# Kernel tuning notes

Hardware: AMD Instinct MI355X
Metric: run time of the kernel (lower is better)

## Reference

```python
import jax, jax.numpy as jnp
import numpy as np
import math

B, T, M, C, H = 4, 1024, 256, 512, 8
HD = C // H
NEG = -1e30


def setup_inputs() -> dict:
    key = jax.random.key(0)
    ks = jax.random.split(key, 16)
    s = 1.0 / math.sqrt(C)
    inp = {
        'x': jax.random.normal(ks[0], (B, T, C), jnp.float32),
        'y': jax.random.normal(ks[1], (B, M, C), jnp.float32),
        'attn_x_mask': jnp.tril(jnp.ones((T, T), bool))[None, None],  # causal (1,1,T,T)
        'Wqkv_x': jax.random.normal(ks[2], (C, 3 * C), jnp.float32) * s,
        'bqkv_x': jnp.zeros((3 * C,), jnp.float32),
        'Wqkv_y': jax.random.normal(ks[3], (C, 3 * C), jnp.float32) * s,
        'bqkv_y': jnp.zeros((3 * C,), jnp.float32),
        'w4x': jax.random.normal(ks[4], (H, HD), jnp.float32) * math.sqrt(1.0 / C / 3),
        'w4y': jax.random.normal(ks[5], (H, HD), jnp.float32) * math.sqrt(1.0 / C / 3),
        'w4xy': jax.random.normal(ks[6], (H, HD), jnp.float32) * math.sqrt(1.0 / C / 3),
        'Wgs': jax.random.normal(ks[7], (C, C), jnp.float32) * s,
        'bgs': jnp.zeros((C,), jnp.float32),
        'Wgc': jax.random.normal(ks[8], (C, C), jnp.float32) * s,
        'bgc': jnp.zeros((C,), jnp.float32),
        'Wp': jax.random.normal(ks[9], (C, C), jnp.float32) * s,
        'bp': jnp.zeros((C,), jnp.float32),
    }
    return inp


def _heads(t):
    b, n, c = t.shape
    return t.reshape(b, n, H, HD).transpose(0, 2, 1, 3)  # (B,H,N,HD)


def reference(x, y, attn_x_mask, Wqkv_x, bqkv_x, Wqkv_y, bqkv_y,
              w4x, w4y, w4xy, Wgs, bgs, Wgc, bgc, Wp, bp):
    q_x, k_x, v_x = [_heads(t) for t in jnp.split(x @ Wqkv_x + bqkv_x, 3, axis=-1)]
    q_y, k_y, v_y = [_heads(t) for t in jnp.split(y @ Wqkv_y + bqkv_y, 3, axis=-1)]
    scale = 1.0 / math.sqrt(HD)

    # additive bias attention: catt1 (per query-x), catt2 (per key-y), catt3 (bilinear)
    catt1 = jnp.einsum('bhtd,hd->bht', q_x, w4x)[..., :, None]          # (B,H,T,1)
    catt2 = jnp.einsum('bhmd,hd->bhm', q_y, w4y)[:, :, None, :]          # (B,H,1,M)
    catt3 = jnp.einsum('bhtd,bhmd->bhtm', q_x * w4xy[None, :, None, :], k_y) * scale
    catt = catt1 + catt2 + catt3                                         # (B,H,T,M)

    catt_x2y = jax.nn.softmax(catt, axis=-1)
    catt_y2x = jax.nn.softmax(catt, axis=-2)

    cval_x2y = jnp.einsum('bhtm,bhmd->bhtd', catt_x2y, v_y)
    cval_x2y = cval_x2y.transpose(0, 2, 1, 3).reshape(B, T, C)

    # product-of-attentions: (T,M) @ (M,T) -> (T,T)
    chain = jnp.einsum('bhtm,bhsm->bhts', catt_x2y, catt_y2x) * (1.0 / math.sqrt(M))
    chain = jnp.where(attn_x_mask, chain, NEG)
    chain = jax.nn.softmax(chain, axis=-1)
    cval_y2x = jnp.einsum('bhts,bhsd->bhtd', chain, v_x)
    cval_y2x = cval_y2x.transpose(0, 2, 1, 3).reshape(B, T, C)

    cval = cval_x2y + cval_y2x + x

    # masked self-attention
    satt = jnp.einsum('bhtd,bhsd->bhts', q_x, k_x) * scale
    satt = jnp.where(attn_x_mask, satt, NEG)
    satt = jax.nn.softmax(satt, axis=-1)
    sval = jnp.einsum('bhts,bhsd->bhtd', satt, v_x).transpose(0, 2, 1, 3).reshape(B, T, C)

    sgate = jax.nn.sigmoid(sval @ Wgs + bgs)
    cgate = jax.nn.sigmoid(cval @ Wgc + bgc)
    out = (sgate * cval + cgate * sval) @ Wp + bp
    return out
```

## Files before the change

kernel.cpp:

```cpp
#include <hip/hip_runtime.h>
#include <hip/hip_bf16.h>

typedef __hip_bfloat16 bf16;
using f4 = __attribute__((ext_vector_type(4))) float;
using s8 = __attribute__((ext_vector_type(8))) short;
using s4 = __attribute__((ext_vector_type(4))) short;

__device__ __forceinline__ void storeOut(float* p, float v) { *p = v; }
__device__ __forceinline__ void storeOut(bf16* p, float v) { *p = __float2bfloat16(v); }
__device__ __forceinline__ short bfs(float x) { return __builtin_bit_cast(short, __float2bfloat16(x)); }

constexpr int B_ = 4, T_ = 1024, M_ = 256, C_ = 512, H_ = 8, HD_ = 64, C3_ = 1536;

#define MFMA16(a, b, c) __builtin_amdgcn_mfma_f32_16x16x32_bf16((a), (b), (c), 0, 0, 0)

__global__ __launch_bounds__(256) void prep_kernel(
    const float* __restrict__ Wqkv_x, const float* __restrict__ Wqkv_y,
    const float* __restrict__ Wgs, const float* __restrict__ Wgc, const float* __restrict__ Wp,
    const float* __restrict__ x, const float* __restrict__ y,
    bf16* __restrict__ WT_x, bf16* __restrict__ WT_y, bf16* __restrict__ WT_gs,
    bf16* __restrict__ WT_gc, bf16* __restrict__ WT_p,
    bf16* __restrict__ x_bf, bf16* __restrict__ y_bf)
{
    __shared__ float Ls[64][65];
    const int tid = threadIdx.x;
    const int bid = blockIdx.x;
    if (bid < 576) {
        const float* W; bf16* WT; int N, t;
        if (bid < 192)      { W = Wqkv_x; WT = WT_x;  N = C3_; t = bid; }
        else if (bid < 384) { W = Wqkv_y; WT = WT_y;  N = C3_; t = bid - 192; }
        else if (bid < 448) { W = Wgs;    WT = WT_gs; N = C_;  t = bid - 384; }
        else if (bid < 512) { W = Wgc;    WT = WT_gc; N = C_;  t = bid - 448; }
        else                { W = Wp;     WT = WT_p;  N = C_;  t = bid - 512; }
        const int K = C_;
        const int tw = N >> 6;
        const int n0 = (t % tw) * 64, k0 = (t / tw) * 64;
        for (int i = tid; i < 1024; i += 256) {
            int kr = i >> 4, ng = i & 15;
            float4 v = *(const float4*)&W[(size_t)(k0 + kr) * N + n0 + ng * 4];
            Ls[ng * 4 + 0][kr] = v.x; Ls[ng * 4 + 1][kr] = v.y;
            Ls[ng * 4 + 2][kr] = v.z; Ls[ng * 4 + 3][kr] = v.w;
        }
        __syncthreads();
        for (int i = tid; i < 512; i += 256) {
            int n = i >> 3, kg = i & 7;
            s8 r;
            #pragma unroll
            for (int j = 0; j < 8; ++j) r[j] = bfs(Ls[n][kg * 8 + j]);
            *(s8*)&WT[(size_t)(n0 + n) * K + k0 + kg * 8] = r;
        }
    } else if (bid < 1600) {
        int i = (bid - 576) * 2048 + tid * 8;
        s8 r;
        #pragma unroll
        for (int j = 0; j < 8; ++j) r[j] = bfs(x[i + j]);
        *(s8*)&x_bf[i] = r;
    } else {
        int i = (bid - 1600) * 2048 + tid * 8;
        s8 r;
        #pragma unroll
        for (int j = 0; j < 8; ++j) r[j] = bfs(y[i + j]);
        *(s8*)&y_bf[i] = r;
    }
}

__global__ __launch_bounds__(256) void qwcatt_kernel(
    const bf16* __restrict__ qkv_x, const bf16* __restrict__ qkv_y,
    const float* __restrict__ w4x, const float* __restrict__ w4y,
    const float* __restrict__ w4xy,
    float* __restrict__ catt1b, float* __restrict__ catt2b, bf16* __restrict__ qw)
{
    const int bid = blockIdx.x;
    const int tid = threadIdx.x;
    if (bid < 160) {
        int i = bid * 256 + tid;
        const bf16* row; const float* w; float* out; int oi;
        if (i < 32768) {
            int bh = i >> 10, t = i & 1023, b = bh >> 3, h = bh & 7;
            row = qkv_x + (size_t)(b * T_ + t) * C3_ + h * HD_;
            w = w4x + h * HD_; out = catt1b; oi = i;
        } else {
            int j = i - 32768;
            int bh = j >> 8, m = j & 255, b = bh >> 3, h = bh & 7;
            row = qkv_y + (size_t)(b * M_ + m) * C3_ + h * HD_;
            w = w4y + h * HD_; out = catt2b; oi = j;
        }
        float s = 0.f;
        #pragma unroll
        for (int d = 0; d < HD_; ++d) s = fmaf(__bfloat162float(row[d]), w[d], s);
        out[oi] = s;
    } else {
        int o = ((bid - 160) * 256 + tid) * 8;
        int row = o >> 9, c = o & 511;
        const bf16* src = qkv_x + (size_t)row * C3_ + c;
        s8 r;
        #pragma unroll
        for (int j = 0; j < 8; ++j) r[j] = bfs(__bfloat162float(src[j]) * w4xy[c + j]);
        *(s8*)&qw[o] = r;
    }
}

template <typename OT>
__global__ __launch_bounds__(256) void gemm_staged_kernel(
    const bf16* __restrict__ A, const bf16* __restrict__ WT, const float* __restrict__ bias,
    OT* __restrict__ Cmat, int N, int K)
{
    __shared__ short Asb[128][72];
    __shared__ short Bsb[64][72];
    const int tid = threadIdx.x;
    const int wave = tid >> 6, lane = tid & 63;
    const int quad = lane >> 4, l16 = lane & 15;
    const int n0 = blockIdx.y * 64, m0 = blockIdx.x * 128;
    f4 acc[2][4];
    #pragma unroll
    for (int mt = 0; mt < 2; ++mt)
        #pragma unroll
        for (int nt = 0; nt < 4; ++nt) acc[mt][nt] = (f4)0.f;

    for (int k0 = 0; k0 < K; k0 += 64) {
        #pragma unroll
        for (int tl = 0; tl < 4; ++tl) {
            int g = tid + tl * 256, row = g >> 3, grp = g & 7;
            *(s8*)&Asb[row][grp * 8] = *(const s8*)&A[(size_t)(m0 + row) * K + k0 + grp * 8];
        }
        #pragma unroll
        for (int tl = 0; tl < 2; ++tl) {
            int g = tid + tl * 256, n = g >> 3, grp = g & 7;
            *(s8*)&Bsb[n][grp * 8] = *(const s8*)&WT[(size_t)(n0 + n) * K + k0 + grp * 8];
        }
        __syncthreads();
        #pragma unroll
        for (int ks = 0; ks < 2; ++ks) {
            s8 a0 = *(const s8*)&Asb[wave * 32 + l16][ks * 32 + quad * 8];
            s8 a1 = *(const s8*)&Asb[wave * 32 + 16 + l16][ks * 32 + quad * 8];
            #pragma unroll
            for (int nt = 0; nt < 4; ++nt) {
                s8 bv = *(const s8*)&Bsb[nt * 16 + l16][ks * 32 + quad * 8];
                acc[0][nt] = MFMA16(a0, bv, acc[0][nt]);
                acc[1][nt] = MFMA16(a1, bv, acc[1][nt]);
            }
        }
        __syncthreads();
    }
    #pragma unroll
    for (int mt = 0; mt < 2; ++mt)
        #pragma unroll
        for (int nt = 0; nt < 4; ++nt) {
            int col = n0 + nt * 16 + l16;
            float bb = bias[col];
            #pragma unroll
            for (int reg = 0; reg < 4; ++reg) {
                int row = m0 + wave * 32 + mt * 16 + quad * 4 + reg;
                storeOut(&Cmat[(size_t)row * N + col], acc[mt][nt][reg] + bb);
            }
        }
}

__global__ __launch_bounds__(256) void catt3_kernel(
    const bf16* __restrict__ qw, const bf16* __restrict__ qkv_y,
    const float* __restrict__ catt1, const float* __restrict__ catt2,
    float* __restrict__ catt, float* __restrict__ psum)
{
    __shared__ float redc[4][64];
    const int tid = threadIdx.x;
    const int wave = tid >> 6, lane = tid & 63;
    const int quad = lane >> 4, l16 = lane & 15;
    const int bh = blockIdx.x, b = bh >> 3, h = bh & 7;
    const int m0 = blockIdx.y * 64, t0 = blockIdx.z * 64;
    f4 sc[4];
    #pragma unroll
    for (int nt = 0; nt < 4; ++nt) sc[nt] = (f4)0.f;
    const bf16* ap = qw + (size_t)(b * T_ + t0 + wave * 16 + l16) * C_ + h * HD_ + quad * 8;
    const bf16* bp = qkv_y + (size_t)(b * M_ + m0 + l16) * C3_ + C_ + h * HD_ + quad * 8;
    #pragma unroll
    for (int k0 = 0; k0 < 64; k0 += 32) {
        s8 a = *(const s8*)(ap + k0);
        #pragma unroll
        for (int nt = 0; nt < 4; ++nt) {
            s8 bv = *(const s8*)(bp + (size_t)nt * 16 * C3_ + k0);
            sc[nt] = MFMA16(a, bv, sc[nt]);
        }
    }
    float csloc[4];
    #pragma unroll
    for (int nt = 0; nt < 4; ++nt) {
        int m = m0 + nt * 16 + l16;
        float c2 = catt2[bh * M_ + m];
        float es = 0.f;
        #pragma unroll
        for (int reg = 0; reg < 4; ++reg) {
            int t = t0 + wave * 16 + quad * 4 + reg;
            float v = sc[nt][reg] * 0.125f + catt1[bh * T_ + t] + c2;
            catt[((size_t)bh * T_ + t) * M_ + m] = v;
            es += __expf(v);
        }
        es += __shfl_xor(es, 16);
        es += __shfl_xor(es, 32);
        csloc[nt] = es;
    }
    if (quad == 0) {
        #pragma unroll
        for (int nt = 0; nt < 4; ++nt) redc[wave][nt * 16 + l16] = csloc[nt];
    }
    __syncthreads();
    if (tid < 64) {
        float s = redc[0][tid] + redc[1][tid] + redc[2][tid] + redc[3][tid];
        psum[((size_t)bh * 16 + (t0 >> 6)) * M_ + m0 + tid] = s;
    }
}

__global__ __launch_bounds__(256) void colfin_vtrans_kernel(
    const float* __restrict__ psum, float* __restrict__ colinv,
    const bf16* __restrict__ qkv_x, const bf16* __restrict__ qkv_y,
    bf16* __restrict__ vTx, bf16* __restrict__ vTy)
{
    __shared__ short Ls[64][68];
    const int tid = threadIdx.x;
    int bid = blockIdx.x;
    if (bid < 32) {
        const int bh = bid, m = tid;
        float s = 0.f;
        #pragma unroll
        for (int ch = 0; ch < 16; ++ch) s += psum[(bh * 16 + ch) * M_ + m];
        colinv[bh * M_ + m] = 1.f / s;
        return;
    }
    bid -= 32;
    const bf16* qkv; bf16* vT; int Nrows, bh, t0;
    if (bid < 512) { qkv = qkv_x; vT = vTx; Nrows = T_; bh = bid >> 4; t0 = (bid & 15) * 64; }
    else { bid -= 512; qkv = qkv_y; vT = vTy; Nrows = M_; bh = bid >> 2; t0 = (bid & 3) * 64; }
    const int b = bh >> 3, h = bh & 7;
    for (int i = tid; i < 4096; i += 256) {
        int tl = i >> 6, d = i & 63;
        Ls[d][tl] = __builtin_bit_cast(short,
            qkv[(size_t)(b * Nrows + t0 + tl) * C3_ + 2 * C_ + h * HD_ + d]);
    }
    __syncthreads();
    for (int i = tid; i < 4096; i += 256) {
        int d = i >> 6, tl = i & 63;
        vT[((size_t)bh * 64 + d) * Nrows + t0 + tl] = __builtin_bit_cast(bf16, Ls[d][tl]);
    }
}

__global__ __launch_bounds__(256) void rowsoft_kernel(
    const float* __restrict__ catt, const float* __restrict__ colinv,
    bf16* __restrict__ x2y, bf16* __restrict__ y2x)
{
    const int wave = threadIdx.x >> 6, lane = threadIdx.x & 63;
    const int row = blockIdx.x * 4 + wave;
    const int bh = row >> 10;
    const float* p = catt + (size_t)row * M_;
    float e[4];
    float s = 0.f;
    #pragma unroll
    for (int j = 0; j < 4; ++j) { e[j] = __expf(p[j * 64 + lane]); s += e[j]; }
    for (int off = 1; off < 64; off <<= 1) s += __shfl_xor(s, off);
    float inv = 1.f / s;
    #pragma unroll
    for (int j = 0; j < 4; ++j) {
        int m = j * 64 + lane;
        x2y[(size_t)row * M_ + m] = __float2bfloat16(e[j] * inv);
        y2x[(size_t)row * M_ + m] = __float2bfloat16(e[j] * colinv[bh * M_ + m]);
    }
}

__global__ __launch_bounds__(512) void flash6_kernel(
    const bf16* __restrict__ x2y, const bf16* __restrict__ y2x,
    const bf16* __restrict__ vTx, const bf16* __restrict__ vTy,
    const bf16* __restrict__ qkv_x, const float* __restrict__ x,
    float* __restrict__ cval, bf16* __restrict__ cval_bf,
    float* __restrict__ sval, bf16* __restrict__ sval_bf)
{
    __shared__ short Kc[64][264];
    __shared__ short Ksf[64][72];
    __shared__ short Vb[64][72];
    __shared__ short Ps[8][16][68];
    const int tid = threadIdx.x;
    const int wave = tid >> 6, lane = tid & 63;
    const int quad = lane >> 4, l16 = lane & 15;
    const int bh = blockIdx.x, b = bh >> 3, h = bh & 7;
    const int p = blockIdx.y;
    const int jt = (wave < 4) ? p : (15 - p);
    const int rb = jt * 64 + (wave & 3) * 16;
    const int nst = 16 - p;

    s8 qc[8], qs[2];
    {
        const bf16* qp = x2y + (size_t)(bh * T_ + rb + l16) * M_ + quad * 8;
        #pragma unroll
        for (int f = 0; f < 8; ++f) qc[f] = *(const s8*)(qp + f * 32);
        const bf16* qsp = qkv_x + (size_t)(b * T_ + rb + l16) * C3_ + h * HD_ + quad * 8;
        qs[0] = *(const s8*)qsp;
        qs[1] = *(const s8*)(qsp + 32);
    }

    f4 ocv[4];
    #pragma unroll
    for (int dt = 0; dt < 4; ++dt) ocv[dt] = (f4)0.f;
    {
        const bf16* vb = vTy + (size_t)(bh * 64 + l16) * M_ + quad * 8;
        #pragma unroll
        for (int f = 0; f < 8; ++f)
            #pragma unroll
            for (int dt = 0; dt < 4; ++dt) {
                s8 bv = *(const s8*)(vb + (size_t)dt * 16 * M_ + f * 32);
                ocv[dt] = MFMA16(qc[f], bv, ocv[dt]);
            }
    }

    f4 oc[4], os_[4];
    float lc[4] = {0.f, 0.f, 0.f, 0.f}, ls_[4] = {0.f, 0.f, 0.f, 0.f};
    #pragma unroll
    for (int dt = 0; dt < 4; ++dt) { oc[dt] = (f4)0.f; os_[dt] = (f4)0.f; }

    #pragma unroll
    for (int tl = 0; tl < 4; ++tl) {
        int g = tid + tl * 512, row = g >> 5, grp = g & 31;
        *(s8*)&Kc[row][grp * 8] = *(const s8*)&y2x[(size_t)(bh * T_ + row) * M_ + grp * 8];
    }
    {
        int row = tid >> 3, grp = tid & 7;
        *(s8*)&Ksf[row][grp * 8] =
            *(const s8*)&qkv_x[(size_t)(b * T_ + row) * C3_ + C_ + h * HD_ + grp * 8];
        *(s8*)&Vb[row][grp * 8] = *(const s8*)&vTx[(size_t)(bh * 64 + row) * T_ + grp * 8];
    }
    __syncthreads();

    for (int st = 0; st < nst; ++st) {
        const int s0 = st * 64;
        const bool pf = (st + 1) < nst;
        s8 kcp[4], ksp, vp;
        if (pf) {
            const int sn = s0 + 64;
            #pragma unroll
            for (int tl = 0; tl < 4; ++tl) {
                int g = tid + tl * 512, row = g >> 5, grp = g & 31;
                kcp[tl] = *(const s8*)&y2x[(size_t)(bh * T_ + sn + row) * M_ + grp * 8];
            }
            int row = tid >> 3, grp = tid & 7;
            ksp = *(const s8*)&qkv_x[(size_t)(b * T_ + sn + row) * C3_ + C_ + h * HD_ + grp * 8];
            vp = *(const s8*)&vTx[(size_t)(bh * 64 + row) * T_ + sn + grp * 8];
        }
        if (st <= jt) {
            f4 sc[4];
            #pragma unroll
            for (int nt = 0; nt < 4; ++nt) sc[nt] = (f4)0.f;
            #pragma unroll
            for (int f = 0; f < 8; ++f)
                #pragma unroll
                for (int nt = 0; nt < 4; ++nt) {
                    s8 bv = *(const s8*)&Kc[nt * 16 + l16][f * 32 + quad * 8];
                    sc[nt] = MFMA16(qc[f], bv, sc[nt]);
                }
            f4 ss[4];
            #pragma unroll
            for (int nt = 0; nt < 4; ++nt) ss[nt] = (f4)0.f;
            #pragma unroll
            for (int f = 0; f < 2; ++f)
                #pragma unroll
                for (int nt = 0; nt < 4; ++nt) {
                    s8 bv = *(const s8*)&Ksf[nt * 16 + l16][f * 32 + quad * 8];
                    ss[nt] = MFMA16(qs[f], bv, ss[nt]);
                }
            #pragma unroll
            for (int reg = 0; reg < 4; ++reg) {
                const int t_g = rb + quad * 4 + reg;
                #pragma unroll
                for (int nt = 0; nt < 4; ++nt) {
                    float pv = (s0 + nt * 16 + l16 <= t_g) ? __expf(sc[nt][reg] * (1.f / 16.f)) : 0.f;
                    lc[reg] += pv;
                    Ps[wave][quad * 4 + reg][nt * 16 + l16] = bfs(pv);
                }
            }
            #pragma unroll
            for (int ks = 0; ks < 2; ++ks) {
                const short* pp = &Ps[wave][l16][ks * 32 + quad * 8];
                s4 alo = *(const s4*)pp;
                s4 ahi = *(const s4*)(pp + 4);
                s8 a;
                a[0] = alo[0]; a[1] = alo[1]; a[2] = alo[2]; a[3] = alo[3];
                a[4] = ahi[0]; a[5] = ahi[1]; a[6] = ahi[2]; a[7] = ahi[3];
                #pragma unroll
                for (int dt = 0; dt < 4; ++dt) {
                    s8 bv = *(const s8*)&Vb[dt * 16 + l16][ks * 32 + quad * 8];
                    oc[dt] = MFMA16(a, bv, oc[dt]);
                }
            }
            #pragma unroll
            for (int reg = 0; reg < 4; ++reg) {
                const int t_g = rb + quad * 4 + reg;
                #pragma unroll
                for (int nt = 0; nt < 4; ++nt) {
                    float pv = (s0 + nt * 16 + l16 <= t_g) ? __expf(ss[nt][reg] * 0.125f) : 0.f;
                    ls_[reg] += pv;
                    Ps[wave][quad * 4 + reg][nt * 16 + l16] = bfs(pv);
                }
            }
            #pragma unroll
            for (int ks = 0; ks < 2; ++ks) {
                const short* pp = &Ps[wave][l16][ks * 32 + quad * 8];
                s4 alo = *(const s4*)pp;
                s4 ahi = *(const s4*)(pp + 4);
                s8 a;
                a[0] = alo[0]; a[1] = alo[1]; a[2] = alo[2]; a[3] = alo[3];
                a[4] = ahi[0]; a[5] = ahi[1]; a[6] = ahi[2]; a[7] = ahi[3];
                #pragma unroll
                for (int dt = 0; dt < 4; ++dt) {
                    s8 bv = *(const s8*)&Vb[dt * 16 + l16][ks * 32 + quad * 8];
                    os_[dt] = MFMA16(a, bv, os_[dt]);
                }
            }
        }
        __syncthreads();
        if (pf) {
            #pragma unroll
            for (int tl = 0; tl < 4; ++tl) {
                int g = tid + tl * 512, row = g >> 5, grp = g & 31;
                *(s8*)&Kc[row][grp * 8] = kcp[tl];
            }
            int row = tid >> 3, grp = tid & 7;
            *(s8*)&Ksf[row][grp * 8] = ksp;
            *(s8*)&Vb[row][grp * 8] = vp;
        }
        __syncthreads();
    }

    #pragma unroll
    for (int reg = 0; reg < 4; ++reg) {
        float l1 = lc[reg], l2 = ls_[reg];
        l1 += __shfl_xor(l1, 1); l1 += __shfl_xor(l1, 2);
        l1 += __shfl_xor(l1, 4); l1 += __shfl_xor(l1, 8);
        l2 += __shfl_xor(l2, 1); l2 += __shfl_xor(l2, 2);
        l2 += __shfl_xor(l2, 4); l2 += __shfl_xor(l2, 8);
        const float i1 = 1.f / l1, i2 = 1.f / l2;
        const int t = rb + quad * 4 + reg;
        #pragma unroll
        for (int dt = 0; dt < 4; ++dt) {
            size_t idx = (size_t)(b * T_ + t) * C_ + h * HD_ + dt * 16 + l16;
            float cv = ocv[dt][reg] + oc[dt][reg] * i1 + x[idx];
            cval[idx] = cv;
            cval_bf[idx] = __float2bfloat16(cv);
            float sv = os_[dt][reg] * i2;
            sval[idx] = sv;
            sval_bf[idx] = __float2bfloat16(sv);
        }
    }
}

__global__ __launch_bounds__(256) void gatefuse_kernel(
    const bf16* __restrict__ svalb, const bf16* __restrict__ cvalb,
    const bf16* __restrict__ WTgs, const bf16* __restrict__ WTgc,
    const float* __restrict__ bgs, const float* __restrict__ bgc,
    const float* __restrict__ cval, const float* __restrict__ sval,
    bf16* __restrict__ gated)
{
    __shared__ short Sb[128][72], Cb[128][72], W1b[64][72], W2b[64][72];
    const int tid = threadIdx.x;
    const int wave = tid >> 6, lane = tid & 63;
    const int quad = lane >> 4, l16 = lane & 15;
    const int n0 = blockIdx.y * 64, m0 = blockIdx.x * 128;
    f4 aS[2][4], aC[2][4];
    #pragma unroll
    for (int mt = 0; mt < 2; ++mt)
        #pragma unroll
        for (int nt = 0; nt < 4; ++nt) { aS[mt][nt] = (f4)0.f; aC[mt][nt] = (f4)0.f; }

    for (int k0 = 0; k0 < C_; k0 += 64) {
        #pragma unroll
        for (int tl = 0; tl < 4; ++tl) {
            int g = tid + tl * 256, row = g >> 3, grp = g & 7;
            *(s8*)&Sb[row][grp * 8] = *(const s8*)&svalb[(size_t)(m0 + row) * C_ + k0 + grp * 8];
            *(s8*)&Cb[row][grp * 8] = *(const s8*)&cvalb[(size_t)(m0 + row) * C_ + k0 + grp * 8];
        }
        #pragma unroll
        for (int tl = 0; tl < 2; ++tl) {
            int g = tid + tl * 256, n = g >> 3, grp = g & 7;
            *(s8*)&W1b[n][grp * 8] = *(const s8*)&WTgs[(size_t)(n0 + n) * C_ + k0 + grp * 8];
            *(s8*)&W2b[n][grp * 8] = *(const s8*)&WTgc[(size_t)(n0 + n) * C_ + k0 + grp * 8];
        }
        __syncthreads();
        #pragma unroll
        for (int ks = 0; ks < 2; ++ks) {
            s8 s0f = *(const s8*)&Sb[wave * 32 + l16][ks * 32 + quad * 8];
            s8 s1f = *(const s8*)&Sb[wave * 32 + 16 + l16][ks * 32 + quad * 8];
            s8 c0f = *(const s8*)&Cb[wave * 32 + l16][ks * 32 + quad * 8];
            s8 c1f = *(const s8*)&Cb[wave * 32 + 16 + l16][ks * 32 + quad * 8];
            #pragma unroll
            for (int nt = 0; nt < 4; ++nt) {
                s8 w1 = *(const s8*)&W1b[nt * 16 + l16][ks * 32 + quad * 8];
                s8 w2 = *(const s8*)&W2b[nt * 16 + l16][ks * 32 + quad * 8];
                aS[0][nt] = MFMA16(s0f, w1, aS[0][nt]);
                aS[1][nt] = MFMA16(s1f, w1, aS[1][nt]);
                aC[0][nt] = MFMA16(c0f, w2, aC[0][nt]);
                aC[1][nt] = MFMA16(c1f, w2, aC[1][nt]);
            }
        }
        __syncthreads();
    }
    #pragma unroll
    for (int mt = 0; mt < 2; ++mt)
        #pragma unroll
        for (int nt = 0; nt < 4; ++nt) {
            int col = n0 + nt * 16 + l16;
            float b1 = bgs[col], b2 = bgc[col];
            #pragma unroll
            for (int reg = 0; reg < 4; ++reg) {
                int row = m0 + wave * 32 + mt * 16 + quad * 4 + reg;
                size_t idx = (size_t)row * C_ + col;
                float gs = 1.f / (1.f + __expf(-(aS[mt][nt][reg] + b1)));
                float gc = 1.f / (1.f + __expf(-(aC[mt][nt][reg] + b2)));
                gated[idx] = __float2bfloat16(gs * cval[idx] + gc * sval[idx]);
            }
        }
}

extern "C" void kernel_launch(void* const* d_in, const int* in_sizes, int n_in,
                              void* d_out, int out_size, void* d_ws, size_t ws_size,
                              hipStream_t stream)
{
    const float* x      = (const float*)d_in[0];
    const float* y      = (const float*)d_in[1];
    const float* Wqkv_x = (const float*)d_in[3];
    const float* bqkv_x = (const float*)d_in[4];
    const float* Wqkv_y = (const float*)d_in[5];
    const float* bqkv_y = (const float*)d_in[6];
    const float* w4x    = (const float*)d_in[7];
    const float* w4y    = (const float*)d_in[8];
    const float* w4xy   = (const float*)d_in[9];
    const float* Wgs    = (const float*)d_in[10];
    const float* bgs    = (const float*)d_in[11];
    const float* Wgc    = (const float*)d_in[12];
    const float* bgc    = (const float*)d_in[13];
    const float* Wp     = (const float*)d_in[14];
    const float* bp     = (const float*)d_in[15];

    float* ws = (float*)d_ws;
    bf16*  qkv_x_bf = (bf16*)(ws + 0);
    bf16*  qkv_y_bf = (bf16*)(ws + 3145728);
    float* catt     = ws + 3932160;
    bf16*  gated_bf = (bf16*)(ws + 3932160);
    bf16*  cval_bf  = (bf16*)(ws + 5242880);
    bf16*  x2y_bf   = (bf16*)(ws + 12320768);
    bf16*  x_bf     = x2y_bf;
    bf16*  y_bf     = (bf16*)(ws + 13369344);
    bf16*  y2x_bf   = (bf16*)(ws + 16515072);
    bf16*  vTx_bf   = (bf16*)(ws + 20709376);
    bf16*  vTy_bf   = (bf16*)(ws + 21757952);
    float* cval     = ws + 22020096;
    float* psum_    = cval;
    float* sval     = ws + 24117248;
    bf16*  qw_bf    = (bf16*)(ws + 26214400);
    bf16*  sval_bf  = qw_bf;
    bf16*  WT_x     = (bf16*)(ws + 27262976);
    bf16*  WT_y     = (bf16*)(ws + 27656192);
    bf16*  WT_gs    = (bf16*)(ws + 28049408);
    bf16*  WT_gc    = (bf16*)(ws + 28180480);
    bf16*  WT_p     = (bf16*)(ws + 28311552);
    float* catt1b   = ws + 28442624;
    float* catt2b   = ws + 28475392;
    float* colinv   = ws + 28483584;

    prep_kernel<<<1856, 256, 0, stream>>>(
        Wqkv_x, Wqkv_y, Wgs, Wgc, Wp, x, y,
        WT_x, WT_y, WT_gs, WT_gc, WT_p, x_bf, y_bf);

    gemm_staged_kernel<bf16><<<dim3(32, 24), 256, 0, stream>>>(x_bf, WT_x, bqkv_x, qkv_x_bf, C3_, C_);
    gemm_staged_kernel<bf16><<<dim3(8, 24), 256, 0, stream>>>(y_bf, WT_y, bqkv_y, qkv_y_bf, C3_, C_);

    qwcatt_kernel<<<1184, 256, 0, stream>>>(
        qkv_x_bf, qkv_y_bf, w4x, w4y, w4xy, catt1b, catt2b, qw_bf);
    catt3_kernel<<<dim3(32, 4, 16), 256, 0, stream>>>(qw_bf, qkv_y_bf, catt1b, catt2b, catt, psum_);

    colfin_vtrans_kernel<<<672, 256, 0, stream>>>(psum_, colinv, qkv_x_bf, qkv_y_bf, vTx_bf, vTy_bf);

    rowsoft_kernel<<<8192, 256, 0, stream>>>(catt, colinv, x2y_bf, y2x_bf);

    flash6_kernel<<<dim3(32, 8), 512, 0, stream>>>(
        x2y_bf, y2x_bf, vTx_bf, vTy_bf, qkv_x_bf, x, cval, cval_bf, sval, sval_bf);

    gatefuse_kernel<<<dim3(32, 8), 256, 0, stream>>>(
        sval_bf, cval_bf, WT_gs, WT_gc, bgs, bgc, cval, sval, gated_bf);

    gemm_staged_kernel<float><<<dim3(32, 8), 256, 0, stream>>>(
        gated_bf, WT_p, bp, (float*)d_out, C_, C_);
}
```

Before: 231.4 us.

## Fuse row softmax into catt3 and derive y2x from normalized x2y

The catt3 kernel now computes the full 256-wide row per block, applies exp, row-normalizes and writes bf16 x2y directly plus row sums, alongside the column partial sums. This removes the fp32 catt intermediate write and re-read. A new lightweight vectorized kernel rebuilds y2x as x2y * rowsum * colinv. The catt3 grid shrinks (fewer, larger blocks with more registers), and reconstructing y2x from the bf16-rounded x2y adds a small precision loss.

```diff
diff --git a/kernel.cpp b/kernel.cpp
--- a/kernel.cpp
+++ b/kernel.cpp
@@ -156,57 +156,82 @@
         }
 }
 
-__global__ __launch_bounds__(256) void catt3_kernel(
+__global__ __launch_bounds__(256) void catt3r_kernel(
     const bf16* __restrict__ qw, const bf16* __restrict__ qkv_y,
     const float* __restrict__ catt1, const float* __restrict__ catt2,
-    float* __restrict__ catt, float* __restrict__ psum)
-{
-    __shared__ float redc[4][64];
+    bf16* __restrict__ x2y, float* __restrict__ rowsum_, float* __restrict__ psum)
+{
+    __shared__ float redc[4][256];
     const int tid = threadIdx.x;
     const int wave = tid >> 6, lane = tid & 63;
     const int quad = lane >> 4, l16 = lane & 15;
     const int bh = blockIdx.x, b = bh >> 3, h = bh & 7;
-    const int m0 = blockIdx.y * 64, t0 = blockIdx.z * 64;
-    f4 sc[4];
-    #pragma unroll
-    for (int nt = 0; nt < 4; ++nt) sc[nt] = (f4)0.f;
+    const int t0 = blockIdx.y * 64;
+    f4 sc[4][4];
+    #pragma unroll
+    for (int mt = 0; mt < 4; ++mt)
+        #pragma unroll
+        for (int nt = 0; nt < 4; ++nt) sc[mt][nt] = (f4)0.f;
+
     const bf16* ap = qw + (size_t)(b * T_ + t0 + wave * 16 + l16) * C_ + h * HD_ + quad * 8;
-    const bf16* bp = qkv_y + (size_t)(b * M_ + m0 + l16) * C3_ + C_ + h * HD_ + quad * 8;
-    #pragma unroll
-    for (int k0 = 0; k0 < 64; k0 += 32) {
-        s8 a = *(const s8*)(ap + k0);
+    s8 a0 = *(const s8*)ap;
+    s8 a1 = *(const s8*)(ap + 32);
+    const bf16* bp = qkv_y + (size_t)(b * M_ + l16) * C3_ + C_ + h * HD_ + quad * 8;
+    #pragma unroll
+    for (int mt = 0; mt < 4; ++mt)
         #pragma unroll
         for (int nt = 0; nt < 4; ++nt) {
-            s8 bv = *(const s8*)(bp + (size_t)nt * 16 * C3_ + k0);
-            sc[nt] = MFMA16(a, bv, sc[nt]);
-        }
-    }
-    float csloc[4];
-    #pragma unroll
-    for (int nt = 0; nt < 4; ++nt) {
-        int m = m0 + nt * 16 + l16;
-        float c2 = catt2[bh * M_ + m];
-        float es = 0.f;
-        #pragma unroll
-        for (int reg = 0; reg < 4; ++reg) {
-            int t = t0 + wave * 16 + quad * 4 + reg;
-            float v = sc[nt][reg] * 0.125f + catt1[bh * T_ + t] + c2;
-            catt[((size_t)bh * T_ + t) * M_ + m] = v;
-            es += __expf(v);
-        }
-        es += __shfl_xor(es, 16);
-        es += __shfl_xor(es, 32);
-        csloc[nt] = es;
-    }
-    if (quad == 0) {
-        #pragma unroll
-        for (int nt = 0; nt < 4; ++nt) redc[wave][nt * 16 + l16] = csloc[nt];
-    }
+            const bf16* bq = bp + (size_t)(mt * 64 + nt * 16) * C3_;
+            sc[mt][nt] = MFMA16(a0, *(const s8*)bq, sc[mt][nt]);
+            sc[mt][nt] = MFMA16(a1, *(const s8*)(bq + 32), sc[mt][nt]);
+        }
+
+    float c1[4];
+    #pragma unroll
+    for (int reg = 0; reg < 4; ++reg)
+        c1[reg] = catt1[bh * T_ + t0 + wave * 16 + quad * 4 + reg];
+    #pragma unroll
+    for (int mt = 0; mt < 4; ++mt)
+        #pragma unroll
+        for (int nt = 0; nt < 4; ++nt) {
+            float c2 = catt2[bh * M_ + mt * 64 + nt * 16 + l16];
+            #pragma unroll
+            for (int reg = 0; reg < 4; ++reg)
+                sc[mt][nt][reg] = __expf(sc[mt][nt][reg] * 0.125f + c1[reg] + c2);
+        }
+
+    #pragma unroll
+    for (int reg = 0; reg < 4; ++reg) {
+        float rs = 0.f;
+        #pragma unroll
+        for (int mt = 0; mt < 4; ++mt)
+            #pragma unroll
+            for (int nt = 0; nt < 4; ++nt) rs += sc[mt][nt][reg];
+        rs += __shfl_xor(rs, 1); rs += __shfl_xor(rs, 2);
+        rs += __shfl_xor(rs, 4); rs += __shfl_xor(rs, 8);
+        const int t = t0 + wave * 16 + quad * 4 + reg;
+        if (l16 == 0) rowsum_[bh * T_ + t] = rs;
+        const float ri = 1.f / rs;
+        #pragma unroll
+        for (int mt = 0; mt < 4; ++mt)
+            #pragma unroll
+            for (int nt = 0; nt < 4; ++nt)
+                x2y[((size_t)bh * T_ + t) * M_ + mt * 64 + nt * 16 + l16] =
+                    __float2bfloat16(sc[mt][nt][reg] * ri);
+    }
+
+    #pragma unroll
+    for (int mt = 0; mt < 4; ++mt)
+        #pragma unroll
+        for (int nt = 0; nt < 4; ++nt) {
+            float es = sc[mt][nt][0] + sc[mt][nt][1] + sc[mt][nt][2] + sc[mt][nt][3];
+            es += __shfl_xor(es, 16);
+            es += __shfl_xor(es, 32);
+            if (quad == 0) redc[wave][mt * 64 + nt * 16 + l16] = es;
+        }
     __syncthreads();
-    if (tid < 64) {
-        float s = redc[0][tid] + redc[1][tid] + redc[2][tid] + redc[3][tid];
-        psum[((size_t)bh * 16 + (t0 >> 6)) * M_ + m0 + tid] = s;
-    }
+    psum[((size_t)bh * 16 + blockIdx.y) * M_ + tid] =
+        redc[0][tid] + redc[1][tid] + redc[2][tid] + redc[3][tid];
 }
 
 __global__ __launch_bounds__(256) void colfin_vtrans_kernel(
@@ -242,26 +267,22 @@
     }
 }
 
-__global__ __launch_bounds__(256) void rowsoft_kernel(
-    const float* __restrict__ catt, const float* __restrict__ colinv,
-    bf16* __restrict__ x2y, bf16* __restrict__ y2x)
-{
-    const int wave = threadIdx.x >> 6, lane = threadIdx.x & 63;
-    const int row = blockIdx.x * 4 + wave;
-    const int bh = row >> 10;
-    const float* p = catt + (size_t)row * M_;
-    float e[4];
-    float s = 0.f;
-    #pragma unroll
-    for (int j = 0; j < 4; ++j) { e[j] = __expf(p[j * 64 + lane]); s += e[j]; }
-    for (int off = 1; off < 64; off <<= 1) s += __shfl_xor(s, off);
-    float inv = 1.f / s;
-    #pragma unroll
-    for (int j = 0; j < 4; ++j) {
-        int m = j * 64 + lane;
-        x2y[(size_t)row * M_ + m] = __float2bfloat16(e[j] * inv);
-        y2x[(size_t)row * M_ + m] = __float2bfloat16(e[j] * colinv[bh * M_ + m]);
-    }
+__global__ __launch_bounds__(256) void y2xw_kernel(
+    const bf16* __restrict__ x2y, const float* __restrict__ rowsum_,
+    const float* __restrict__ colinv, bf16* __restrict__ y2x)
+{
+    const int i = (blockIdx.x * 256 + threadIdx.x) * 8;
+    const int row = i >> 8, m = i & 255, bh = row >> 10;
+    const float rs = rowsum_[row];
+    s8 v = *(const s8*)&x2y[i];
+    const float4 c0 = *(const float4*)&colinv[bh * M_ + m];
+    const float4 c4 = *(const float4*)&colinv[bh * M_ + m + 4];
+    float ci[8] = {c0.x, c0.y, c0.z, c0.w, c4.x, c4.y, c4.z, c4.w};
+    s8 r;
+    #pragma unroll
+    for (int j = 0; j < 8; ++j)
+        r[j] = bfs(__bfloat162float(__builtin_bit_cast(bf16, v[j])) * rs * ci[j]);
+    *(s8*)&y2x[i] = r;
 }
 
 __global__ __launch_bounds__(512) void flash6_kernel(
@@ -537,7 +558,6 @@
     float* ws = (float*)d_ws;
     bf16*  qkv_x_bf = (bf16*)(ws + 0);
     bf16*  qkv_y_bf = (bf16*)(ws + 3145728);
-    float* catt     = ws + 3932160;
     bf16*  gated_bf = (bf16*)(ws + 3932160);
     bf16*  cval_bf  = (bf16*)(ws + 5242880);
     bf16*  x2y_bf   = (bf16*)(ws + 12320768);
@@ -559,6 +579,7 @@
     float* catt1b   = ws + 28442624;
     float* catt2b   = ws + 28475392;
     float* colinv   = ws + 28483584;
+    float* rowsum_  = ws + 28491776;
 
     prep_kernel<<<1856, 256, 0, stream>>>(
         Wqkv_x, Wqkv_y, Wgs, Wgc, Wp, x, y,
@@ -569,11 +590,13 @@
 
     qwcatt_kernel<<<1184, 256, 0, stream>>>(
         qkv_x_bf, qkv_y_bf, w4x, w4y, w4xy, catt1b, catt2b, qw_bf);
-    catt3_kernel<<<dim3(32, 4, 16), 256, 0, stream>>>(qw_bf, qkv_y_bf, catt1b, catt2b, catt, psum_);
+
+    catt3r_kernel<<<dim3(32, 16), 256, 0, stream>>>(
+        qw_bf, qkv_y_bf, catt1b, catt2b, x2y_bf, rowsum_, psum_);
 
     colfin_vtrans_kernel<<<672, 256, 0, stream>>>(psum_, colinv, qkv_x_bf, qkv_y_bf, vTx_bf, vTy_bf);
 
-    rowsoft_kernel<<<8192, 256, 0, stream>>>(catt, colinv, x2y_bf, y2x_bf);
+    y2xw_kernel<<<4096, 256, 0, stream>>>(x2y_bf, rowsum_, colinv, y2x_bf);
 
     flash6_kernel<<<dim3(32, 8), 512, 0, stream>>>(
         x2y_bf, y2x_bf, vTx_bf, vTy_bf, qkv_x_bf, x, cval, cval_bf, sval, sval_bf);
```

Result: faster. 226.3 us (-2.2%).
